# Optimization experiments

Hardware: AMD Instinct MI355X
Metric: run time of the kernel (lower is better)

The kernel has to match this reference:

```python
import jax, jax.numpy as jnp
import numpy as np

N_NODES = 100000
N_EDGES = 1600000
IN_F = 128
OUT_F = 32
NHEAD = 4
ALPHA = 0.2  # leaky relu negative slope


def setup_inputs() -> dict:
    key = jax.random.key(0)
    k1, k2, k3, k4, k5 = jax.random.split(key, 5)
    x = jax.random.normal(k1, (N_NODES, IN_F), dtype=jnp.float32)
    edge_index = jax.random.randint(k2, (2, N_EDGES), 0, N_NODES, dtype=jnp.int32)
    # glorot-ish init as in reset_parameters
    stdv_w = np.sqrt(6.0 / (IN_F + OUT_F * NHEAD))
    W = jax.random.uniform(k3, (IN_F, OUT_F * NHEAD), minval=-stdv_w, maxval=stdv_w, dtype=jnp.float32)
    stdv_a = np.sqrt(6.0 / (NHEAD + OUT_F))
    a_l = jax.random.uniform(k4, (1, NHEAD, OUT_F), minval=-stdv_a, maxval=stdv_a, dtype=jnp.float32)
    a_r = jax.random.uniform(k5, (1, NHEAD, OUT_F), minval=-stdv_a, maxval=stdv_a, dtype=jnp.float32)
    return {"x": x, "edge_index": edge_index, "W": W, "a_l": a_l, "a_r": a_r}


def reference(x, edge_index, W, a_l, a_r):
    N = x.shape[0]
    # h: [N, nhead, out]
    h = jnp.matmul(x, W).reshape(N, NHEAD, OUT_F)
    h = jnp.nan_to_num(h)
    row, col = edge_index[0], edge_index[1]
    # per-node attention halves: [N, nhead]
    al = (a_l * h).sum(axis=-1)
    ar = (a_r * h).sum(axis=-1)
    # per-edge raw scores: [E, nhead]
    e = jax.nn.leaky_relu(al[row] + ar[col], negative_slope=ALPHA)
    # segment softmax over incoming edges of each destination node (row)
    m = jax.ops.segment_max(e, row, num_segments=N)           # [N, nhead]
    e_exp = jnp.exp(e - m[row])                               # [E, nhead]
    s = jax.ops.segment_sum(e_exp, row, num_segments=N)       # [N, nhead]
    att = e_exp / s[row]                                      # [E, nhead]
    # spmm aggregation per head: out[i] = sum_{(i,j) in E} att_ij * h[j]
    msg = att[:, :, None] * h[col]                            # [E, nhead, out]
    out = jax.ops.segment_sum(msg, row, num_segments=N)       # [N, nhead, out]
    return out.reshape(N, NHEAD * OUT_F)
```

## Files before the change

### kernel.cpp

```cpp
#include <hip/hip_runtime.h>
#include <hip/hip_bf16.h>
#include <string.h>

#define NN 100000
#define NE 1600000
#define INF_ 128
#define OC 128
#define NH 4
#define ALPHA 0.2f
#define LDA 272

#define BSH 9
#define BINW 512
#define NBIN ((NN + BINW - 1) / BINW)
#define CAPB 10240
#define EPT 16
#define EPB (256 * EPT)
#define NPB1 ((NE + EPB - 1) / EPB)
#define CAP2 12288

typedef __bf16 bf16x8 __attribute__((ext_vector_type(8)));
typedef float f32x4 __attribute__((ext_vector_type(4)));
typedef float f32x2 __attribute__((ext_vector_type(2)));

__device__ __forceinline__ float lrelu(float x) {
    return x > 0.0f ? x : ALPHA * x;
}
__device__ __forceinline__ unsigned short f2bf(float f) {
    __hip_bfloat16 b = __float2bfloat16(f);
    unsigned short u; memcpy(&u, &b, 2); return u;
}
__device__ __forceinline__ int sel4(const int4 v, int j) {
    const int lo = (j & 1) ? v.y : v.x;
    const int hi = (j & 1) ? v.w : v.z;
    return (j & 2) ? hi : lo;
}

__global__ __launch_bounds__(256) void k_pre(
    const float* __restrict__ W, __hip_bfloat16* __restrict__ Wt,
    int* __restrict__ bincur) {
    const int i = blockIdx.x * 256 + threadIdx.x;
    const int co = i >> 7, ko = i & 127;
    Wt[i] = __float2bfloat16(W[ko * OC + co]);
    if (blockIdx.x == 0 && threadIdx.x < NBIN)
        bincur[threadIdx.x] = threadIdx.x * CAPB;
}

__global__ __launch_bounds__(256) void k_gp1(
    const float* __restrict__ x, const __hip_bfloat16* __restrict__ Wt,
    const float* __restrict__ a_l, const float* __restrict__ a_r,
    __hip_bfloat16* __restrict__ hb, float* __restrict__ al, float* __restrict__ ar,
    const int* __restrict__ row, const int* __restrict__ col,
    int* __restrict__ bincur, unsigned* __restrict__ tmp) {
    __shared__ __align__(16) char smem[128 * LDA];
    const int tid = threadIdx.x;
    const int m5 = blockIdx.x % 5;

    if (m5 != 4) {
        char* sB = smem;
        const int gb = (blockIdx.x / 5) * 4 + m5;
        const int rowBase = gb * 64;

        for (int i4 = tid; i4 < 2048; i4 += 256) {
            const int c = i4 >> 4, k4 = i4 & 15;
            *(uint4*)(sB + c * LDA + k4 * 16) =
                *(const uint4*)((const char*)Wt + (size_t)c * 256 + k4 * 16);
        }
        __syncthreads();

        const int lane = tid & 63;
        const int w = tid >> 6;
        const int arow = w * 16 + (lane & 15);
        const int grow = rowBase + arow;
        const int growc = (grow < NN) ? grow : (NN - 1);
        const int koff8 = (lane >> 4) * 8;
        const int koff = (lane >> 4) * 16;

        f32x4 acc[8];
#pragma unroll
        for (int n = 0; n < 8; ++n) acc[n] = (f32x4){0.f, 0.f, 0.f, 0.f};

#pragma unroll
        for (int kk = 0; kk < 4; ++kk) {
            const float* xp = x + (size_t)growc * INF_ + kk * 32 + koff8;
            const float4 f0 = *(const float4*)xp;
            const float4 f1 = *(const float4*)(xp + 4);
            union { bf16x8 v; unsigned short u[8]; } au;
            au.u[0] = f2bf(f0.x); au.u[1] = f2bf(f0.y);
            au.u[2] = f2bf(f0.z); au.u[3] = f2bf(f0.w);
            au.u[4] = f2bf(f1.x); au.u[5] = f2bf(f1.y);
            au.u[6] = f2bf(f1.z); au.u[7] = f2bf(f1.w);
#pragma unroll
            for (int n = 0; n < 8; ++n) {
                const int brow = n * 16 + (lane & 15);
                const bf16x8 b = *(const bf16x8*)(sB + brow * LDA + kk * 64 + koff);
                acc[n] = __builtin_amdgcn_mfma_f32_16x16x32_bf16(au.v, b, acc[n], 0, 0, 0);
            }
        }

        const int rbase = rowBase + w * 16 + (lane >> 4) * 4;
#pragma unroll
        for (int n = 0; n < 8; ++n) {
            const int cc = n * 16 + (lane & 15);
#pragma unroll
            for (int r = 0; r < 4; ++r) {
                const int rw = rbase + r;
                if (rw < NN) hb[(size_t)rw * OC + cc] = __float2bfloat16(acc[n][r]);
            }
        }

        float alw[8], arw[8];
#pragma unroll
        for (int n = 0; n < 8; ++n) {
            alw[n] = a_l[n * 16 + (lane & 15)];
            arw[n] = a_r[n * 16 + (lane & 15)];
        }
#pragma unroll
        for (int r = 0; r < 4; ++r) {
            const int rw = rbase + r;
#pragma unroll
            for (int hd = 0; hd < 4; ++hd) {
                float pl = acc[2 * hd][r] * alw[2 * hd] + acc[2 * hd + 1][r] * alw[2 * hd + 1];
                float pr = acc[2 * hd][r] * arw[2 * hd] + acc[2 * hd + 1][r] * arw[2 * hd + 1];
#pragma unroll
                for (int m = 1; m <= 8; m <<= 1) {
                    pl += __shfl_xor(pl, m);
                    pr += __shfl_xor(pr, m);
                }
                if ((lane & 15) == hd && rw < NN) {
                    al[rw * NH + hd] = pl;
                    ar[rw * NH + hd] = pr;
                }
            }
        }
    } else {
        int* h     = (int*)smem;
        int* gbase = h + NBIN;
        int* lcur  = gbase + NBIN;
        const int pb = blockIdx.x / 5;
        const int t = tid;
        for (int i = t; i < NBIN; i += 256) { h[i] = 0; lcur[i] = 0; }
        __syncthreads();

        const int e0 = pb * EPB + t * EPT;
        int r[EPT], c[EPT];
        if (e0 + EPT <= NE) {
#pragma unroll
            for (int q = 0; q < EPT / 4; ++q) {
                const int4 rv = *(const int4*)&row[e0 + q * 4];
                const int4 cv = *(const int4*)&col[e0 + q * 4];
                r[q*4+0] = rv.x; r[q*4+1] = rv.y; r[q*4+2] = rv.z; r[q*4+3] = rv.w;
                c[q*4+0] = cv.x; c[q*4+1] = cv.y; c[q*4+2] = cv.z; c[q*4+3] = cv.w;
            }
        } else {
#pragma unroll
            for (int i = 0; i < EPT; ++i) {
                const int e = e0 + i;
                r[i] = (e < NE) ? row[e] : -1;
                c[i] = (e < NE) ? col[e] : 0;
            }
        }
#pragma unroll
        for (int i = 0; i < EPT; ++i)
            if (r[i] >= 0) atomicAdd(&h[r[i] >> BSH], 1);
        __syncthreads();
        for (int i = t; i < NBIN; i += 256)
            if (h[i]) gbase[i] = atomicAdd(&bincur[i], h[i]);
        __syncthreads();
#pragma unroll
        for (int i = 0; i < EPT; ++i) {
            if (r[i] < 0) continue;
            const int b = r[i] >> BSH;
            const int pos = atomicAdd(&lcur[b], 1);
            tmp[gbase[b] + pos] =
                ((unsigned)(r[i] & (BINW - 1)) << 17) | (unsigned)c[i];
        }
    }
}

__global__ __launch_bounds__(256) void k_part2(
    const unsigned* __restrict__ tmp, const int* __restrict__ bincur,
    int2* __restrict__ nodeinfo, int* __restrict__ cols_s) {
    __shared__ unsigned stage[CAP2];
    __shared__ int h[BINW], ps[256], cur[BINW];
    const int b = blockIdx.x, t = threadIdx.x;
    const int node0 = b * BINW;
    const int gs = b * CAPB;
    const int cnt = bincur[b] - gs;
    for (int i = t; i < BINW; i += 256) h[i] = 0;
    __syncthreads();
    for (int j = t; j < cnt; j += 256) {
        const unsigned p = tmp[gs + j];
        if (j < CAP2) stage[j] = p;
        atomicAdd(&h[p >> 17], 1);
    }
    __syncthreads();
    const int a0 = h[2 * t], a1 = h[2 * t + 1];
    ps[t] = a0 + a1;
    __syncthreads();
    for (int o = 1; o < 256; o <<= 1) {
        const int add = (t >= o) ? ps[t - o] : 0;
        __syncthreads();
        ps[t] += add;
        __syncthreads();
    }
    const int ex = ps[t] - a0 - a1 + gs;
    cur[2 * t] = ex;
    cur[2 * t + 1] = ex + a0;
    if (node0 + 2 * t < NN)     nodeinfo[node0 + 2 * t]     = make_int2(ex, a0);
    if (node0 + 2 * t + 1 < NN) nodeinfo[node0 + 2 * t + 1] = make_int2(ex + a0, a1);
    __syncthreads();
    for (int j = t; j < cnt; j += 256) {
        const unsigned p = (j < CAP2) ? stage[j] : tmp[gs + j];
        const int pos = atomicAdd(&cur[p >> 17], 1);
        cols_s[pos] = (int)(p & 0x1FFFFu);
    }
}

__global__ __launch_bounds__(256) void k_agg(
    const int2* __restrict__ nodeinfo, const int* __restrict__ cols_s,
    const float* __restrict__ al, const float* __restrict__ ar,
    const __hip_bfloat16* __restrict__ hb, float* __restrict__ out) {
    const int w = threadIdx.x >> 6;
    const int lane = threadIdx.x & 63;
    const int g = lane >> 4;
    const int sl = lane & 15;
    const int node = blockIdx.x * 16 + w * 4 + g;
    if (node >= NN) return;

    const int2 info = nodeinfo[node];
    const int start = info.x;
    const int deg = info.y;
    const int hsel = sl >> 2;
    const int je = sl >> 2;
    const int sh = sl & 3;
    const int sbase = lane & 48;
    const float al_sh = al[node * NH + sh];
    const char* hrow = (const char*)hb + sl * 16;

    f32x2 a0 = {0.f, 0.f}, a1 = {0.f, 0.f}, a2 = {0.f, 0.f}, a3 = {0.f, 0.f};
    float ssum = 0.f;

    int4 cA = *(const int4*)(cols_s + start);
    int4 cB = *(const int4*)(cols_s + start + 4);

    for (int kk = 0; kk < deg; kk += 8) {
        const int rem = deg - kk;
        const int4 cA2 = *(const int4*)(cols_s + start + kk + 8);
        const int4 cB2 = *(const int4*)(cols_s + start + kk + 12);

        float wvA = 0.f, wvB = 0.f;
        if (je < rem) {
            const int c = sel4(cA, je);
            wvA = __expf(lrelu(al_sh + ar[c * NH + sh]));
        }
        if (je + 4 < rem) {
            const int c = sel4(cB, je);
            wvB = __expf(lrelu(al_sh + ar[c * NH + sh]));
        }

        int c_[8] = {cA.x, cA.y, cA.z, cA.w, cB.x, cB.y, cB.z, cB.w};
#pragma unroll
        for (int j = 0; j < 8; ++j)
            if (j >= rem) c_[j] = 0;

#pragma unroll
        for (int j = 0; j < 8; ++j) {
            const float wj = __shfl(j < 4 ? wvA : wvB, sbase + (j & 3) * 4 + hsel);
            const uint4 v = *(const uint4*)(hrow + (size_t)c_[j] * 256);
            a0 += wj * (f32x2){__uint_as_float(v.x << 16), __uint_as_float(v.x & 0xffff0000u)};
            a1 += wj * (f32x2){__uint_as_float(v.y << 16), __uint_as_float(v.y & 0xffff0000u)};
            a2 += wj * (f32x2){__uint_as_float(v.z << 16), __uint_as_float(v.z & 0xffff0000u)};
            a3 += wj * (f32x2){__uint_as_float(v.w << 16), __uint_as_float(v.w & 0xffff0000u)};
            ssum += wj;
        }
        cA = cA2; cB = cB2;
    }

    const float inv = (ssum > 0.f) ? 1.0f / ssum : 0.f;
    float4 o0, o1;
    o0.x = a0.x * inv; o0.y = a0.y * inv; o0.z = a1.x * inv; o0.w = a1.y * inv;
    o1.x = a2.x * inv; o1.y = a2.y * inv; o1.z = a3.x * inv; o1.w = a3.y * inv;
    float* dst = out + (size_t)node * OC + sl * 8;
    *(float4*)dst = o0;
    *(float4*)(dst + 4) = o1;
}

extern "C" void kernel_launch(void* const* d_in, const int* in_sizes, int n_in,
                              void* d_out, int out_size, void* d_ws, size_t ws_size,
                              hipStream_t stream) {
    const float* x    = (const float*)d_in[0];
    const int*   ei   = (const int*)d_in[1];
    const float* W    = (const float*)d_in[2];
    const float* a_l  = (const float*)d_in[3];
    const float* a_r  = (const float*)d_in[4];
    float* out = (float*)d_out;

    const int* row = ei;
    const int* col = ei + NE;

    char* ws = (char*)d_ws;
    __hip_bfloat16* hb = (__hip_bfloat16*)ws;   ws += (size_t)NN * OC * 2;
    __hip_bfloat16* Wt = (__hip_bfloat16*)ws;   ws += (size_t)INF_ * OC * 2;
    float*    al      = (float*)ws;             ws += (size_t)NN * NH * 4;
    float*    ar      = (float*)ws;             ws += (size_t)NN * NH * 4;
    int*      cols_s  = (int*)ws;               ws += (size_t)NBIN * CAPB * 4;
    unsigned* tmp     = (unsigned*)ws;          ws += (size_t)NBIN * CAPB * 4;
    int2*     nodeinfo= (int2*)ws;              ws += (size_t)NN * 8;
    int*      bincur  = (int*)ws;               ws += (size_t)NBIN * 4;

    k_pre<<<64, 256, 0, stream>>>(W, Wt, bincur);
    k_gp1<<<1955, 256, 0, stream>>>(x, Wt, a_l, a_r, hb, al, ar, row, col, bincur, tmp);
    k_part2<<<NBIN, 256, 0, stream>>>(tmp, bincur, nodeinfo, cols_s);
    k_agg<<<(NN + 15) / 16, 256, 0, stream>>>(nodeinfo, cols_s, al, ar, hb, out);
}
```

Baseline: 133.4 us.

## Fold attention vectors into GEMM weights and halve partition bin width

Precomputes W·a_l and W·a_r as eight extra bf16 weight columns, so the attention halves al/ar come out of a ninth MFMA tile. This replaces the per-row shuffle reductions in the GEMM epilogue. Separately, the CSR partition bins shrink from 512 to 256 nodes, which doubles the number of k_part2 blocks and simplifies the scan to one element per thread. The trade-offs are a bf16 rounding of the folded attention weights (slightly different al/ar) and more bin atomics and counters in the partition phase.

```diff
diff --git a/kernel.cpp b/kernel.cpp
--- a/kernel.cpp
+++ b/kernel.cpp
@@ -10,14 +10,14 @@
 #define ALPHA 0.2f
 #define LDA 272
 
-#define BSH 9
-#define BINW 512
+#define BSH 8
+#define BINW 256
 #define NBIN ((NN + BINW - 1) / BINW)
-#define CAPB 10240
+#define CAPB 5120
 #define EPT 16
 #define EPB (256 * EPT)
 #define NPB1 ((NE + EPB - 1) / EPB)
-#define CAP2 12288
+#define CAP2B 6144
 
 typedef __bf16 bf16x8 __attribute__((ext_vector_type(8)));
 typedef float f32x4 __attribute__((ext_vector_type(4)));
@@ -37,22 +37,38 @@
 }
 
 __global__ __launch_bounds__(256) void k_pre(
-    const float* __restrict__ W, __hip_bfloat16* __restrict__ Wt,
+    const float* __restrict__ W, const float* __restrict__ a_l,
+    const float* __restrict__ a_r, __hip_bfloat16* __restrict__ Wt,
     int* __restrict__ bincur) {
-    const int i = blockIdx.x * 256 + threadIdx.x;
-    const int co = i >> 7, ko = i & 127;
-    Wt[i] = __float2bfloat16(W[ko * OC + co]);
-    if (blockIdx.x == 0 && threadIdx.x < NBIN)
-        bincur[threadIdx.x] = threadIdx.x * CAPB;
+    const int t = threadIdx.x;
+    const int b = blockIdx.x;
+    if (b < 64) {
+        const int i = b * 256 + t;
+        const int co = i >> 7, ko = i & 127;
+        Wt[i] = __float2bfloat16(W[ko * OC + co]);
+    } else {
+        const int i = (b - 64) * 256 + t;
+        const int cp = i >> 7, k = i & 127;
+        float v = 0.f;
+        if (cp < 8) {
+            const int hd = cp & 3;
+            const float* av = (cp < 4) ? a_l : a_r;
+#pragma unroll 8
+            for (int j = 0; j < 32; ++j)
+                v += W[k * OC + hd * 32 + j] * av[hd * 32 + j];
+        }
+        Wt[(128 + cp) * 128 + k] = __float2bfloat16(v);
+    }
+    if (b == 0)
+        for (int i = t; i < NBIN; i += 256) bincur[i] = i * CAPB;
 }
 
 __global__ __launch_bounds__(256) void k_gp1(
     const float* __restrict__ x, const __hip_bfloat16* __restrict__ Wt,
-    const float* __restrict__ a_l, const float* __restrict__ a_r,
     __hip_bfloat16* __restrict__ hb, float* __restrict__ al, float* __restrict__ ar,
     const int* __restrict__ row, const int* __restrict__ col,
     int* __restrict__ bincur, unsigned* __restrict__ tmp) {
-    __shared__ __align__(16) char smem[128 * LDA];
+    __shared__ __align__(16) char smem[144 * LDA];
     const int tid = threadIdx.x;
     const int m5 = blockIdx.x % 5;
 
@@ -61,7 +77,7 @@
         const int gb = (blockIdx.x / 5) * 4 + m5;
         const int rowBase = gb * 64;
 
-        for (int i4 = tid; i4 < 2048; i4 += 256) {
+        for (int i4 = tid; i4 < 144 * 16; i4 += 256) {
             const int c = i4 >> 4, k4 = i4 & 15;
             *(uint4*)(sB + c * LDA + k4 * 16) =
                 *(const uint4*)((const char*)Wt + (size_t)c * 256 + k4 * 16);
@@ -76,9 +92,9 @@
         const int koff8 = (lane >> 4) * 8;
         const int koff = (lane >> 4) * 16;
 
-        f32x4 acc[8];
-#pragma unroll
-        for (int n = 0; n < 8; ++n) acc[n] = (f32x4){0.f, 0.f, 0.f, 0.f};
+        f32x4 acc[9];
+#pragma unroll
+        for (int n = 0; n < 9; ++n) acc[n] = (f32x4){0.f, 0.f, 0.f, 0.f};
 
 #pragma unroll
         for (int kk = 0; kk < 4; ++kk) {
@@ -91,7 +107,7 @@
             au.u[4] = f2bf(f1.x); au.u[5] = f2bf(f1.y);
             au.u[6] = f2bf(f1.z); au.u[7] = f2bf(f1.w);
 #pragma unroll
-            for (int n = 0; n < 8; ++n) {
+            for (int n = 0; n < 9; ++n) {
                 const int brow = n * 16 + (lane & 15);
                 const bf16x8 b = *(const bf16x8*)(sB + brow * LDA + kk * 64 + koff);
                 acc[n] = __builtin_amdgcn_mfma_f32_16x16x32_bf16(au.v, b, acc[n], 0, 0, 0);
@@ -108,29 +124,14 @@
                 if (rw < NN) hb[(size_t)rw * OC + cc] = __float2bfloat16(acc[n][r]);
             }
         }
-
-        float alw[8], arw[8];
-#pragma unroll
-        for (int n = 0; n < 8; ++n) {
-            alw[n] = a_l[n * 16 + (lane & 15)];
-            arw[n] = a_r[n * 16 + (lane & 15)];
-        }
-#pragma unroll
-        for (int r = 0; r < 4; ++r) {
-            const int rw = rbase + r;
-#pragma unroll
-            for (int hd = 0; hd < 4; ++hd) {
-                float pl = acc[2 * hd][r] * alw[2 * hd] + acc[2 * hd + 1][r] * alw[2 * hd + 1];
-                float pr = acc[2 * hd][r] * arw[2 * hd] + acc[2 * hd + 1][r] * arw[2 * hd + 1];
-#pragma unroll
-                for (int m = 1; m <= 8; m <<= 1) {
-                    pl += __shfl_xor(pl, m);
-                    pr += __shfl_xor(pr, m);
-                }
-                if ((lane & 15) == hd && rw < NN) {
-                    al[rw * NH + hd] = pl;
-                    ar[rw * NH + hd] = pr;
-                }
+        const int cp = lane & 15;
+        if (cp < 8) {
+            const int hd = cp & 3;
+            float* dst = (cp < 4) ? al : ar;
+#pragma unroll
+            for (int r = 0; r < 4; ++r) {
+                const int rw = rbase + r;
+                if (rw < NN) dst[rw * NH + hd] = acc[8][r];
             }
         }
     } else {
@@ -181,37 +182,35 @@
 __global__ __launch_bounds__(256) void k_part2(
     const unsigned* __restrict__ tmp, const int* __restrict__ bincur,
     int2* __restrict__ nodeinfo, int* __restrict__ cols_s) {
-    __shared__ unsigned stage[CAP2];
-    __shared__ int h[BINW], ps[256], cur[BINW];
+    __shared__ unsigned stage[CAP2B];
+    __shared__ int h[BINW], ts[256], cur[BINW];
     const int b = blockIdx.x, t = threadIdx.x;
     const int node0 = b * BINW;
     const int gs = b * CAPB;
     const int cnt = bincur[b] - gs;
-    for (int i = t; i < BINW; i += 256) h[i] = 0;
+    h[t] = 0;
     __syncthreads();
     for (int j = t; j < cnt; j += 256) {
         const unsigned p = tmp[gs + j];
-        if (j < CAP2) stage[j] = p;
+        if (j < CAP2B) stage[j] = p;
         atomicAdd(&h[p >> 17], 1);
     }
     __syncthreads();
-    const int a0 = h[2 * t], a1 = h[2 * t + 1];
-    ps[t] = a0 + a1;
+    const int v = h[t];
+    ts[t] = v;
     __syncthreads();
     for (int o = 1; o < 256; o <<= 1) {
-        const int add = (t >= o) ? ps[t - o] : 0;
-        __syncthreads();
-        ps[t] += add;
-        __syncthreads();
-    }
-    const int ex = ps[t] - a0 - a1 + gs;
-    cur[2 * t] = ex;
-    cur[2 * t + 1] = ex + a0;
-    if (node0 + 2 * t < NN)     nodeinfo[node0 + 2 * t]     = make_int2(ex, a0);
-    if (node0 + 2 * t + 1 < NN) nodeinfo[node0 + 2 * t + 1] = make_int2(ex + a0, a1);
+        const int add = (t >= o) ? ts[t - o] : 0;
+        __syncthreads();
+        ts[t] += add;
+        __syncthreads();
+    }
+    const int ex = ts[t] - v + gs;
+    cur[t] = ex;
+    if (node0 + t < NN) nodeinfo[node0 + t] = make_int2(ex, v);
     __syncthreads();
     for (int j = t; j < cnt; j += 256) {
-        const unsigned p = (j < CAP2) ? stage[j] : tmp[gs + j];
+        const unsigned p = (j < CAP2B) ? stage[j] : tmp[gs + j];
         const int pos = atomicAdd(&cur[p >> 17], 1);
         cols_s[pos] = (int)(p & 0x1FFFFu);
     }
@@ -301,7 +300,7 @@
 
     char* ws = (char*)d_ws;
     __hip_bfloat16* hb = (__hip_bfloat16*)ws;   ws += (size_t)NN * OC * 2;
-    __hip_bfloat16* Wt = (__hip_bfloat16*)ws;   ws += (size_t)INF_ * OC * 2;
+    __hip_bfloat16* Wt = (__hip_bfloat16*)ws;   ws += (size_t)144 * 128 * 2;
     float*    al      = (float*)ws;             ws += (size_t)NN * NH * 4;
     float*    ar      = (float*)ws;             ws += (size_t)NN * NH * 4;
     int*      cols_s  = (int*)ws;               ws += (size_t)NBIN * CAPB * 4;
@@ -309,8 +308,8 @@
     int2*     nodeinfo= (int2*)ws;              ws += (size_t)NN * 8;
     int*      bincur  = (int*)ws;               ws += (size_t)NBIN * 4;
 
-    k_pre<<<64, 256, 0, stream>>>(W, Wt, bincur);
-    k_gp1<<<1955, 256, 0, stream>>>(x, Wt, a_l, a_r, hb, al, ar, row, col, bincur, tmp);
+    k_pre<<<72, 256, 0, stream>>>(W, a_l, a_r, Wt, bincur);
+    k_gp1<<<1955, 256, 0, stream>>>(x, Wt, hb, al, ar, row, col, bincur, tmp);
     k_part2<<<NBIN, 256, 0, stream>>>(tmp, bincur, nodeinfo, cols_s);
     k_agg<<<(NN + 15) / 16, 256, 0, stream>>>(nodeinfo, cols_s, al, ar, hb, out);
 }
```

After: 125.3 us. -6.1%, faster.
